# Optimization experiments

Hardware: AMD Instinct MI355X
Metric: run time of the kernel (lower is better)

The kernel has to match this reference:

```python
import jax, jax.numpy as jnp
import numpy as np

N = 10000      # nodes
E = 160000     # directed edges (script symmetrizes; random here)
IN = 512       # input feature dim
H = 512        # hidden dim
OUT = 16       # classes


def setup_inputs() -> dict:
    key = jax.random.key(0)
    ks = jax.random.split(key, 8)
    x = jax.random.normal(ks[0], (N, IN), dtype=jnp.float32)
    edge_index = jax.random.randint(ks[1], (2, E), 0, N, dtype=jnp.int64)

    def glorot(k, shape):
        lim = np.sqrt(6.0 / (shape[0] + shape[1])).astype(np.float32)
        return jax.random.uniform(k, shape, dtype=jnp.float32, minval=-lim, maxval=lim)

    W1 = glorot(ks[2], (IN, H));  b1 = jnp.zeros((H,), jnp.float32)
    W2 = glorot(ks[3], (H, H));   b2 = jnp.zeros((H,), jnp.float32)
    Wl = glorot(ks[4], (H, OUT)); bl = jnp.zeros((OUT,), jnp.float32)
    return {"x": x, "edge_index": edge_index,
            "W1": W1, "b1": b1, "W2": W2, "b2": b2, "Wl": Wl, "bl": bl}


def gcn_conv(x, edge_index, W, b):
    """PyG GCNConv: D^{-1/2}(A+I)D^{-1/2} X W + b, unit edge weights."""
    n = x.shape[0]
    src, dst = edge_index[0], edge_index[1]
    h = x @ W                                   # [N, H] transform first (in<=out path)
    # degree with self-loops (all edge weights = 1)
    deg = jnp.zeros((n,), h.dtype).at[dst].add(1.0) + 1.0
    dinv = jax.lax.rsqrt(deg)                   # deg >= 1, no inf handling needed
    norm = dinv[src] * dinv[dst]                # [E]
    msgs = norm[:, None] * h[src]               # [E, H] gather + scale
    agg = jax.ops.segment_sum(msgs, dst, num_segments=n)
    agg = agg + (dinv * dinv)[:, None] * h      # self-loop contribution
    return agg + b


def reference(x, edge_index, W1, b1, W2, b2, Wl, bl):
    h = jax.nn.relu(gcn_conv(x, edge_index, W1, b1))
    # dropout is identity at inference
    h = jax.nn.relu(gcn_conv(h, edge_index, W2, b2))
    return h @ Wl + bl                          # [N, OUT] logits
```

## Files before the change

### kernel.cpp

```cpp
#include <hip/hip_runtime.h>
#include <stdint.h>

#define NF 512
#define OUT_F 16
#define PAD_DEG 128
#define GBM 64
#define GBN 128
#define NCHUNK 4

typedef __attribute__((ext_vector_type(8))) _Float16 half8;
typedef __attribute__((ext_vector_type(4))) _Float16 half4v;
typedef __attribute__((ext_vector_type(4))) float f32x4;

#define GLOAD_LDS16(g, l) \
  __builtin_amdgcn_global_load_lds((const __attribute__((address_space(1))) unsigned int*)(g), \
                                   (__attribute__((address_space(3))) unsigned int*)(l), 16, 0, 0)


__global__ void edge_prep_kernel(const int* __restrict__ src, const int* __restrict__ dst,
                                 int* __restrict__ counts, int* __restrict__ src_pad, int E) {
    int e = blockIdx.x * blockDim.x + threadIdx.x;
    if (e < E) {
        int d = dst[e];
        int slot = atomicAdd(&counts[d], 1);
        if (slot < PAD_DEG) src_pad[(size_t)d * PAD_DEG + slot] = src[e];
    }
}


__global__ __launch_bounds__(256) void convert_w_kernel(
    const float* __restrict__ W1, const float* __restrict__ W2,
    _Float16* __restrict__ T1, _Float16* __restrict__ T2) {
    __shared__ float tile[64][65];
    int id = blockIdx.x;
    const float* W;  _Float16* WT;
    if (id < 64) { W = W1; WT = T1; }
    else         { W = W2; WT = T2; id -= 64; }
    int k0 = (id & 7) * 64, n0 = (id >> 3) * 64;
    int tr = threadIdx.x >> 4;
    int tc4 = (threadIdx.x & 15) * 4;
#pragma unroll
    for (int i = 0; i < 4; ++i) {
        int r = tr + i * 16;
        float4 v = *(const float4*)(W + (size_t)(k0 + r) * NF + n0 + tc4);
        tile[r][tc4 + 0] = v.x; tile[r][tc4 + 1] = v.y;
        tile[r][tc4 + 2] = v.z; tile[r][tc4 + 3] = v.w;
    }
    __syncthreads();
#pragma unroll
    for (int i = 0; i < 4; ++i) {
        int n = tr + i * 16;
        half4v hv;
#pragma unroll
        for (int j = 0; j < 4; ++j) hv[j] = (_Float16)tile[tc4 + j][n];
        *(half4v*)(WT + (size_t)(n0 + n) * NF + k0 + tc4) = hv;
    }
}


__global__ __launch_bounds__(256) void convert_x_kernel(
    const float* __restrict__ x, _Float16* __restrict__ x16, int Nreal, int Mp) {
    int idx = blockIdx.x * 256 + threadIdx.x;
    int row = idx >> 6;
    int c8 = (idx & 63) * 8;
    if (row >= Mp) return;
    half8 hv = {0, 0, 0, 0, 0, 0, 0, 0};
    if (row < Nreal) {
        float4 v0 = *(const float4*)(x + (size_t)row * NF + c8);
        float4 v1 = *(const float4*)(x + (size_t)row * NF + c8 + 4);
        hv[0] = (_Float16)v0.x; hv[1] = (_Float16)v0.y;
        hv[2] = (_Float16)v0.z; hv[3] = (_Float16)v0.w;
        hv[4] = (_Float16)v1.x; hv[5] = (_Float16)v1.y;
        hv[6] = (_Float16)v1.z; hv[7] = (_Float16)v1.w;
    }
    *(half8*)(x16 + (size_t)row * NF + c8) = hv;
}


__global__ __launch_bounds__(256) void gemm_mfma_kernel(
    const _Float16* __restrict__ A, const _Float16* __restrict__ BT,
    const int* __restrict__ counts, _Float16* __restrict__ Ch) {
    __shared__ _Float16 lds[GBM * 64 + GBN * 64];
    _Float16* As = lds;
    _Float16* Bs = lds + GBM * 64;

    int t = threadIdx.x;
    int w = t >> 6, lane = t & 63, l15 = lane & 15, q = lane >> 4;
    int m0 = (blockIdx.x >> 2) * GBM;
    int n0 = (blockIdx.x & 3) * GBN;
    int wr = w >> 1, wc = w & 1;

    int gr = lane >> 3;
    int gc = ((lane & 7) ^ (gr & 7)) * 8;
    const _Float16* Ag0 = A + (size_t)(m0 + w * 8 + gr) * NF + gc;
    const _Float16* Ag1 = A + (size_t)(m0 + 32 + w * 8 + gr) * NF + gc;
    const _Float16* Bg0 = BT + (size_t)(n0 + w * 8 + gr) * NF + gc;
    const _Float16* Bg1 = BT + (size_t)(n0 + 32 + w * 8 + gr) * NF + gc;
    const _Float16* Bg2 = BT + (size_t)(n0 + 64 + w * 8 + gr) * NF + gc;
    const _Float16* Bg3 = BT + (size_t)(n0 + 96 + w * 8 + gr) * NF + gc;
    _Float16* As_d0 = As + (w * 8) * 64;
    _Float16* As_d1 = As + (32 + w * 8) * 64;
    _Float16* Bs_d0 = Bs + (w * 8) * 64;
    _Float16* Bs_d1 = Bs + (32 + w * 8) * 64;
    _Float16* Bs_d2 = Bs + (64 + w * 8) * 64;
    _Float16* Bs_d3 = Bs + (96 + w * 8) * 64;

    f32x4 acc[2][4] = {};

    for (int k0 = 0; k0 < NF; k0 += 64) {
        GLOAD_LDS16(Ag0 + k0, As_d0);
        GLOAD_LDS16(Ag1 + k0, As_d1);
        GLOAD_LDS16(Bg0 + k0, Bs_d0);
        GLOAD_LDS16(Bg1 + k0, Bs_d1);
        GLOAD_LDS16(Bg2 + k0, Bs_d2);
        GLOAD_LDS16(Bg3 + k0, Bs_d3);
        __syncthreads();

        int key = l15 & 7;
#pragma unroll
        for (int kk = 0; kk < 2; ++kk) {
            int ch = ((kk * 4 + q) ^ key) * 8;
            half8 a[2], b[4];
#pragma unroll
            for (int r = 0; r < 2; ++r)
                a[r] = *(const half8*)(As + (wr * 32 + r * 16 + l15) * 64 + ch);
#pragma unroll
            for (int c = 0; c < 4; ++c)
                b[c] = *(const half8*)(Bs + (wc * 64 + c * 16 + l15) * 64 + ch);
#pragma unroll
            for (int r = 0; r < 2; ++r)
#pragma unroll
                for (int c = 0; c < 4; ++c)
                    acc[r][c] = __builtin_amdgcn_mfma_f32_16x16x32_f16(a[r], b[c], acc[r][c], 0, 0, 0);
        }
        __syncthreads();
    }

#pragma unroll
    for (int r = 0; r < 2; ++r)
#pragma unroll
        for (int i = 0; i < 4; ++i) {
            int row = m0 + wr * 32 + r * 16 + q * 4 + i;
            float dv = rsqrtf((float)counts[row] + 1.0f);
#pragma unroll
            for (int c = 0; c < 4; ++c) {
                int col = n0 + wc * 64 + c * 16 + l15;
                Ch[(size_t)row * NF + col] = (_Float16)(acc[r][c][i] * dv);
            }
        }
}


__global__ __launch_bounds__(256) void agg_kernel(
    const _Float16* __restrict__ hb, const int* __restrict__ counts,
    const int* __restrict__ src_pad, const float* __restrict__ bias,
    _Float16* __restrict__ out_h, int Mreal) {
    int chunk = blockIdx.x & (NCHUNK - 1);
    int node = (blockIdx.x >> 2) * 4 + (threadIdx.x >> 6);
    int lane = threadIdx.x & 63;
    int g = lane >> 4;
    int j = lane & 15;
    int f8 = chunk * 128 + j * 8;
    size_t obase = (size_t)node * NF + f8;

    if (node >= Mreal) {
        if (g == 0) {
            half8 z = {0, 0, 0, 0, 0, 0, 0, 0};
            *(half8*)(out_h + obase) = z;
        }
        return;
    }

    int cntr = counts[node];
    int cnt = cntr < PAD_DEG ? cntr : PAD_DEG;
    const int* sp = src_pad + (size_t)node * PAD_DEG;

    float acc[8] = {};
    for (int e = 0; e < cnt; e += 16) {
        int4 s4 = *(const int4*)(sp + e + g * 4);
        int base = e + g * 4;
        int sidx[4] = {s4.x, s4.y, s4.z, s4.w};
#pragma unroll
        for (int tq = 0; tq < 4; ++tq) {
            bool ok = (base + tq) < cnt;
            int srow = ok ? sidx[tq] : node;
            float m = ok ? 1.f : 0.f;
            half8 hv = *(const half8*)(hb + (size_t)srow * NF + f8);
#pragma unroll
            for (int k = 0; k < 8; ++k) acc[k] = fmaf(m, (float)hv[k], acc[k]);
        }
    }

#pragma unroll
    for (int k = 0; k < 8; ++k) {
        acc[k] += __shfl_xor(acc[k], 16);
        acc[k] += __shfl_xor(acc[k], 32);
    }

    if (g != 0) return;

    half8 sv = *(const half8*)(hb + obase);
    float dv = rsqrtf((float)cntr + 1.0f);
    half8 o8;
#pragma unroll
    for (int k = 0; k < 8; ++k) {
        float o = fmaxf(fmaf(dv, acc[k] + (float)sv[k], bias[f8 + k]), 0.f);
        o8[k] = (_Float16)o;
    }
    *(half8*)(out_h + obase) = o8;
}


__global__ __launch_bounds__(256) void head_kernel(
    const _Float16* __restrict__ in, const float* __restrict__ Wl,
    const float* __restrict__ bl, float* __restrict__ out, int M) {
    __shared__ float Ws[NF * OUT_F];
    int tid = threadIdx.x;
    for (int i = tid; i < NF * OUT_F; i += 256) Ws[i] = Wl[i];
    __syncthreads();
    int node = blockIdx.x * 16 + (tid >> 4);
    int o = tid & 15;
    if (node >= M) return;
    const half8* row8 = (const half8*)(in + (size_t)node * NF);
    float acc = 0.f;
#pragma unroll 2
    for (int k8 = 0; k8 < NF / 8; ++k8) {
        half8 hv = row8[k8];
        int kb = k8 * 8;
#pragma unroll
        for (int u = 0; u < 8; ++u)
            acc = fmaf((float)hv[u], Ws[(kb + u) * OUT_F + o], acc);
    }
    out[(size_t)node * OUT_F + o] = acc + bl[o];
}


extern "C" void kernel_launch(void* const* d_in, const int* in_sizes, int n_in,
                              void* d_out, int out_size, void* d_ws, size_t ws_size,
                              hipStream_t stream) {
    const float* x  = (const float*)d_in[0];
    const int* eidx = (const int*)d_in[1];
    const float* W1 = (const float*)d_in[2];
    const float* b1 = (const float*)d_in[3];
    const float* W2 = (const float*)d_in[4];
    const float* b2 = (const float*)d_in[5];
    const float* Wl = (const float*)d_in[6];
    const float* bl = (const float*)d_in[7];

    int N = in_sizes[0] / NF;
    int E = in_sizes[1] / 2;
    int Mp = (N + GBM - 1) & ~(GBM - 1);
    const int* src = eidx;
    const int* dst = eidx + E;

    char* p = (char*)d_ws;
    auto carve = [&](size_t bytes) -> void* {
        void* r = (void*)p;
        p += (bytes + 255) & ~(size_t)255;
        return r;
    };
    _Float16* hbuf = (_Float16*)carve((size_t)Mp * NF * sizeof(_Float16));
    _Float16* abuf = (_Float16*)carve((size_t)Mp * NF * sizeof(_Float16));
    _Float16* W1T  = (_Float16*)carve((size_t)NF * NF * sizeof(_Float16));
    _Float16* W2T  = (_Float16*)carve((size_t)NF * NF * sizeof(_Float16));
    int* counts    = (int*)carve((size_t)Mp * sizeof(int));
    int* src_pad   = (int*)carve((size_t)N * PAD_DEG * sizeof(int));

    hipMemsetAsync(counts, 0, (size_t)Mp * sizeof(int), stream);

    edge_prep_kernel<<<dim3((E + 255) / 256), dim3(256), 0, stream>>>(src, dst, counts, src_pad, E);
    convert_w_kernel<<<dim3(128), dim3(256), 0, stream>>>(W1, W2, W1T, W2T);
    convert_x_kernel<<<dim3(Mp / 4), dim3(256), 0, stream>>>(x, abuf, N, Mp);

    dim3 gg((Mp / GBM) * (NF / GBN));
    dim3 ga(Mp);

    gemm_mfma_kernel<<<gg, dim3(256), 0, stream>>>(abuf, W1T, counts, hbuf);
    agg_kernel<<<ga, dim3(256), 0, stream>>>(hbuf, counts, src_pad, b1, abuf, N);
    gemm_mfma_kernel<<<gg, dim3(256), 0, stream>>>(abuf, W2T, counts, hbuf);
    agg_kernel<<<ga, dim3(256), 0, stream>>>(hbuf, counts, src_pad, b2, abuf, N);
    head_kernel<<<dim3((N + 15) / 16), dim3(256), 0, stream>>>(abuf, Wl, bl, (float*)d_out, N);
}
```

Measured before the change: 172.6 us.

## Merge prep kernels into one launch and give each wave a full node row

Fuses the edge-prep, weight-convert and x-convert kernels into a single launch that dispatches on block index, saving two kernel launches. Rewrites the aggregation so each 64-lane wave covers all 512 features of one node, walking that node's neighbors serially with a 4-way unrolled gather. This replaces the old split into 4 feature chunks with 4 lane groups reduced by shuffles. It removes the cross-lane reduction and the redundant per-chunk index loads, at the cost of less parallelism per node and a serial per-neighbor chain.

```diff
diff --git a/kernel.cpp b/kernel.cpp
--- a/kernel.cpp
+++ b/kernel.cpp
@@ -6,7 +6,6 @@
 #define PAD_DEG 128
 #define GBM 64
 #define GBN 128
-#define NCHUNK 4
 
 typedef __attribute__((ext_vector_type(8))) _Float16 half8;
 typedef __attribute__((ext_vector_type(4))) _Float16 half4v;
@@ -17,63 +16,64 @@
                                    (__attribute__((address_space(3))) unsigned int*)(l), 16, 0, 0)
 
 
-__global__ void edge_prep_kernel(const int* __restrict__ src, const int* __restrict__ dst,
-                                 int* __restrict__ counts, int* __restrict__ src_pad, int E) {
-    int e = blockIdx.x * blockDim.x + threadIdx.x;
-    if (e < E) {
-        int d = dst[e];
-        int slot = atomicAdd(&counts[d], 1);
-        if (slot < PAD_DEG) src_pad[(size_t)d * PAD_DEG + slot] = src[e];
-    }
-}
-
-
-__global__ __launch_bounds__(256) void convert_w_kernel(
+__global__ __launch_bounds__(256) void prep_kernel(
     const float* __restrict__ W1, const float* __restrict__ W2,
-    _Float16* __restrict__ T1, _Float16* __restrict__ T2) {
+    _Float16* __restrict__ T1, _Float16* __restrict__ T2,
+    const float* __restrict__ x, _Float16* __restrict__ x16,
+    const int* __restrict__ src, const int* __restrict__ dst,
+    int* __restrict__ counts, int* __restrict__ src_pad,
+    int E, int Nreal, int Mp) {
     __shared__ float tile[64][65];
-    int id = blockIdx.x;
-    const float* W;  _Float16* WT;
-    if (id < 64) { W = W1; WT = T1; }
-    else         { W = W2; WT = T2; id -= 64; }
-    int k0 = (id & 7) * 64, n0 = (id >> 3) * 64;
-    int tr = threadIdx.x >> 4;
-    int tc4 = (threadIdx.x & 15) * 4;
-#pragma unroll
-    for (int i = 0; i < 4; ++i) {
-        int r = tr + i * 16;
-        float4 v = *(const float4*)(W + (size_t)(k0 + r) * NF + n0 + tc4);
-        tile[r][tc4 + 0] = v.x; tile[r][tc4 + 1] = v.y;
-        tile[r][tc4 + 2] = v.z; tile[r][tc4 + 3] = v.w;
-    }
-    __syncthreads();
-#pragma unroll
-    for (int i = 0; i < 4; ++i) {
-        int n = tr + i * 16;
-        half4v hv;
-#pragma unroll
-        for (int j = 0; j < 4; ++j) hv[j] = (_Float16)tile[tc4 + j][n];
-        *(half4v*)(WT + (size_t)(n0 + n) * NF + k0 + tc4) = hv;
-    }
-}
-
-
-__global__ __launch_bounds__(256) void convert_x_kernel(
-    const float* __restrict__ x, _Float16* __restrict__ x16, int Nreal, int Mp) {
-    int idx = blockIdx.x * 256 + threadIdx.x;
-    int row = idx >> 6;
-    int c8 = (idx & 63) * 8;
-    if (row >= Mp) return;
-    half8 hv = {0, 0, 0, 0, 0, 0, 0, 0};
-    if (row < Nreal) {
-        float4 v0 = *(const float4*)(x + (size_t)row * NF + c8);
-        float4 v1 = *(const float4*)(x + (size_t)row * NF + c8 + 4);
-        hv[0] = (_Float16)v0.x; hv[1] = (_Float16)v0.y;
-        hv[2] = (_Float16)v0.z; hv[3] = (_Float16)v0.w;
-        hv[4] = (_Float16)v1.x; hv[5] = (_Float16)v1.y;
-        hv[6] = (_Float16)v1.z; hv[7] = (_Float16)v1.w;
-    }
-    *(half8*)(x16 + (size_t)row * NF + c8) = hv;
+    int b = blockIdx.x;
+    int xblocks = Mp / 4;
+
+    if (b < 128) {
+        int id = b;
+        const float* W;  _Float16* WT;
+        if (id < 64) { W = W1; WT = T1; }
+        else         { W = W2; WT = T2; id -= 64; }
+        int k0 = (id & 7) * 64, n0 = (id >> 3) * 64;
+        int tr = threadIdx.x >> 4;
+        int tc4 = (threadIdx.x & 15) * 4;
+#pragma unroll
+        for (int i = 0; i < 4; ++i) {
+            int r = tr + i * 16;
+            float4 v = *(const float4*)(W + (size_t)(k0 + r) * NF + n0 + tc4);
+            tile[r][tc4 + 0] = v.x; tile[r][tc4 + 1] = v.y;
+            tile[r][tc4 + 2] = v.z; tile[r][tc4 + 3] = v.w;
+        }
+        __syncthreads();
+#pragma unroll
+        for (int i = 0; i < 4; ++i) {
+            int n = tr + i * 16;
+            half4v hv;
+#pragma unroll
+            for (int j = 0; j < 4; ++j) hv[j] = (_Float16)tile[tc4 + j][n];
+            *(half4v*)(WT + (size_t)(n0 + n) * NF + k0 + tc4) = hv;
+        }
+    } else if (b < 128 + xblocks) {
+        int idx = (b - 128) * 256 + threadIdx.x;
+        int row = idx >> 6;
+        int c8 = (idx & 63) * 8;
+        if (row >= Mp) return;
+        half8 hv = {0, 0, 0, 0, 0, 0, 0, 0};
+        if (row < Nreal) {
+            float4 v0 = *(const float4*)(x + (size_t)row * NF + c8);
+            float4 v1 = *(const float4*)(x + (size_t)row * NF + c8 + 4);
+            hv[0] = (_Float16)v0.x; hv[1] = (_Float16)v0.y;
+            hv[2] = (_Float16)v0.z; hv[3] = (_Float16)v0.w;
+            hv[4] = (_Float16)v1.x; hv[5] = (_Float16)v1.y;
+            hv[6] = (_Float16)v1.z; hv[7] = (_Float16)v1.w;
+        }
+        *(half8*)(x16 + (size_t)row * NF + c8) = hv;
+    } else {
+        int e = (b - 128 - xblocks) * 256 + threadIdx.x;
+        if (e < E) {
+            int d = dst[e];
+            int slot = atomicAdd(&counts[d], 1);
+            if (slot < PAD_DEG) src_pad[(size_t)d * PAD_DEG + slot] = src[e];
+        }
+    }
 }
 
 
@@ -155,19 +155,14 @@
     const _Float16* __restrict__ hb, const int* __restrict__ counts,
     const int* __restrict__ src_pad, const float* __restrict__ bias,
     _Float16* __restrict__ out_h, int Mreal) {
-    int chunk = blockIdx.x & (NCHUNK - 1);
-    int node = (blockIdx.x >> 2) * 4 + (threadIdx.x >> 6);
+    int node = __builtin_amdgcn_readfirstlane(blockIdx.x * 4 + (threadIdx.x >> 6));
     int lane = threadIdx.x & 63;
-    int g = lane >> 4;
-    int j = lane & 15;
-    int f8 = chunk * 128 + j * 8;
+    int f8 = lane * 8;
     size_t obase = (size_t)node * NF + f8;
 
     if (node >= Mreal) {
-        if (g == 0) {
-            half8 z = {0, 0, 0, 0, 0, 0, 0, 0};
-            *(half8*)(out_h + obase) = z;
-        }
+        half8 z = {0, 0, 0, 0, 0, 0, 0, 0};
+        *(half8*)(out_h + obase) = z;
         return;
     }
 
@@ -175,36 +170,35 @@
     int cnt = cntr < PAD_DEG ? cntr : PAD_DEG;
     const int* sp = src_pad + (size_t)node * PAD_DEG;
 
+    half8 sv = *(const half8*)(hb + obase);
+    float4 b0 = *(const float4*)(bias + f8);
+    float4 b1 = *(const float4*)(bias + f8 + 4);
+
     float acc[8] = {};
-    for (int e = 0; e < cnt; e += 16) {
-        int4 s4 = *(const int4*)(sp + e + g * 4);
-        int base = e + g * 4;
-        int sidx[4] = {s4.x, s4.y, s4.z, s4.w};
-#pragma unroll
-        for (int tq = 0; tq < 4; ++tq) {
-            bool ok = (base + tq) < cnt;
-            int srow = ok ? sidx[tq] : node;
-            float m = ok ? 1.f : 0.f;
-            half8 hv = *(const half8*)(hb + (size_t)srow * NF + f8);
-#pragma unroll
-            for (int k = 0; k < 8; ++k) acc[k] = fmaf(m, (float)hv[k], acc[k]);
-        }
-    }
-
+    int e = 0;
+    for (; e + 3 < cnt; e += 4) {
+        int s0 = sp[e], s1 = sp[e + 1], s2 = sp[e + 2], s3 = sp[e + 3];
+        half8 v0 = *(const half8*)(hb + (size_t)s0 * NF + f8);
+        half8 v1 = *(const half8*)(hb + (size_t)s1 * NF + f8);
+        half8 v2 = *(const half8*)(hb + (size_t)s2 * NF + f8);
+        half8 v3 = *(const half8*)(hb + (size_t)s3 * NF + f8);
+#pragma unroll
+        for (int k = 0; k < 8; ++k)
+            acc[k] += ((float)v0[k] + (float)v1[k]) + ((float)v2[k] + (float)v3[k]);
+    }
+    for (; e < cnt; ++e) {
+        int s = sp[e];
+        half8 v = *(const half8*)(hb + (size_t)s * NF + f8);
+#pragma unroll
+        for (int k = 0; k < 8; ++k) acc[k] += (float)v[k];
+    }
+
+    float dv = rsqrtf((float)cntr + 1.0f);
+    float bb[8] = {b0.x, b0.y, b0.z, b0.w, b1.x, b1.y, b1.z, b1.w};
+    half8 o8;
 #pragma unroll
     for (int k = 0; k < 8; ++k) {
-        acc[k] += __shfl_xor(acc[k], 16);
-        acc[k] += __shfl_xor(acc[k], 32);
-    }
-
-    if (g != 0) return;
-
-    half8 sv = *(const half8*)(hb + obase);
-    float dv = rsqrtf((float)cntr + 1.0f);
-    half8 o8;
-#pragma unroll
-    for (int k = 0; k < 8; ++k) {
-        float o = fmaxf(fmaf(dv, acc[k] + (float)sv[k], bias[f8 + k]), 0.f);
+        float o = fmaxf(fmaf(dv, acc[k] + (float)sv[k], bb[k]), 0.f);
         o8[k] = (_Float16)o;
     }
     *(half8*)(out_h + obase) = o8;
@@ -268,12 +262,13 @@
 
     hipMemsetAsync(counts, 0, (size_t)Mp * sizeof(int), stream);
 
-    edge_prep_kernel<<<dim3((E + 255) / 256), dim3(256), 0, stream>>>(src, dst, counts, src_pad, E);
-    convert_w_kernel<<<dim3(128), dim3(256), 0, stream>>>(W1, W2, W1T, W2T);
-    convert_x_kernel<<<dim3(Mp / 4), dim3(256), 0, stream>>>(x, abuf, N, Mp);
+    int xblocks = Mp / 4;
+    int eblocks = (E + 255) / 256;
+    prep_kernel<<<dim3(128 + xblocks + eblocks), dim3(256), 0, stream>>>(
+        W1, W2, W1T, W2T, x, abuf, src, dst, counts, src_pad, E, N, Mp);
 
     dim3 gg((Mp / GBM) * (NF / GBN));
-    dim3 ga(Mp);
+    dim3 ga(Mp / 4);
 
     gemm_mfma_kernel<<<gg, dim3(256), 0, stream>>>(abuf, W1T, counts, hbuf);
     agg_kernel<<<ga, dim3(256), 0, stream>>>(hbuf, counts, src_pad, b1, abuf, N);
```

Measured after the change: 169.1 us. 2.0% less time.
